# Kernel tuning notes

Hardware: AMD Instinct MI355X
Metric: run time of the kernel (lower is better)

## Reference

```python
import jax, jax.numpy as jnp
import numpy as np
from jax import lax

B, S, I = 256, 16, 64
D = 128
N_ITEMS = 100000
K = 3
PAD_ID = 0
BOS_ID = N_ITEMS
DILATIONS = (1, 2, 4)


def setup_inputs() -> dict:
    key = jax.random.key(0)
    ks = jax.random.split(key, 16)
    item_id = jax.random.randint(ks[0], (B, S, I), 0, N_ITEMS, dtype=jnp.int32)
    eval_from = jax.random.randint(ks[1], (B,), 0, S, dtype=jnp.int32)
    u_type = jax.random.randint(ks[2], (B,), 0, 4, dtype=jnp.int32)
    emb = jax.random.normal(ks[3], (N_ITEMS + 1, D), jnp.float32) * 0.05
    emb = emb.at[PAD_ID].set(0.0)  # padding_idx=0
    kaiming = (2.0 / (D * K)) ** 0.5
    conv_w0 = jax.random.normal(ks[4], (D, D, K), jnp.float32) * kaiming
    conv_w1 = jax.random.normal(ks[5], (D, D, K), jnp.float32) * kaiming
    conv_w2 = jax.random.normal(ks[6], (D, D, K), jnp.float32) * kaiming
    conv_b0 = jnp.zeros((D,), jnp.float32)
    conv_b1 = jnp.zeros((D,), jnp.float32)
    conv_b2 = jnp.zeros((D,), jnp.float32)
    gru_wih = jax.random.normal(ks[7], (3 * D, D), jnp.float32) * 0.05
    gru_whh = jax.random.normal(ks[8], (3 * D, D), jnp.float32) * 0.05
    gru_bih = jax.random.normal(ks[9], (3 * D,), jnp.float32) * 0.05
    gru_bhh = jax.random.normal(ks[10], (3 * D,), jnp.float32) * 0.05
    fus_w = jax.random.normal(ks[11], (D, 2 * D), jnp.float32) * 0.05
    fus_b = jnp.zeros((D,), jnp.float32)
    return {"item_id": item_id, "eval_from": eval_from, "u_type": u_type,
            "emb": emb,
            "conv_w0": conv_w0, "conv_b0": conv_b0,
            "conv_w1": conv_w1, "conv_b1": conv_b1,
            "conv_w2": conv_w2, "conv_b2": conv_b2,
            "gru_wih": gru_wih, "gru_whh": gru_whh,
            "gru_bih": gru_bih, "gru_bhh": gru_bhh,
            "fus_w": fus_w, "fus_b": fus_b}


def reference(item_id, eval_from, u_type, emb,
              conv_w0, conv_b0, conv_w1, conv_b1, conv_w2, conv_b2,
              gru_wih, gru_whh, gru_bih, gru_bhh, fus_w, fus_b):
    item_id = jnp.maximum(item_id, 0)  # clamp_min(0)
    Bc, Sc, Ic = item_id.shape
    convs = ((conv_w0, conv_b0, DILATIONS[0]),
             (conv_w1, conv_b1, DILATIONS[1]),
             (conv_w2, conv_b2, DILATIONS[2]))

    def tcn(x):  # x: [B, T, D] -> [B, T, D]
        h = jnp.transpose(x, (0, 2, 1))  # NCH
        for w, b, dil in convs:
            pad = (K - 1) * dil
            out = lax.conv_general_dilated(
                h, w, window_strides=(1,), padding=[(pad, 0)],
                rhs_dilation=(dil,),
                dimension_numbers=('NCH', 'OIH', 'NCH')) + b[None, :, None]
            h = jax.nn.relu(out + h)
        return jnp.transpose(h, (0, 2, 1))

    def gru_step(h, x):  # h,x: [B, D]
        gi = x @ gru_wih.T + gru_bih
        gh = h @ gru_whh.T + gru_bhh
        ir, iz, inn = jnp.split(gi, 3, axis=-1)
        hr, hz, hn = jnp.split(gh, 3, axis=-1)
        r = jax.nn.sigmoid(ir + hr)
        z = jax.nn.sigmoid(iz + hz)
        n = jnp.tanh(inn + r * hn)
        return (1.0 - z) * n + z * h

    pos = jnp.arange(Ic + 1)
    bos = jnp.full((Bc, 1), BOS_ID, dtype=item_id.dtype)

    def step(h, seq_s):  # seq_s: [B, I]
        lengths = (seq_s != PAD_ID).sum(-1)          # [B]
        max_len = lengths.max()                       # batch-level session max
        seq = jnp.concatenate([bos, seq_s], axis=1)   # [B, I+1], BOS prepended
        valid = pos[None, :] <= max_len               # positions torch keeps
        seq = jnp.where(valid, seq, PAD_ID)
        mask = seq != PAD_ID
        e = emb[seq]                                  # [B, I+1, D] (PAD row is 0)
        tc = tcn(e)
        fin = jnp.concatenate([tc, jnp.broadcast_to(h[:, None, :], tc.shape)], -1)
        reps = fin @ fus_w.T + fus_b                  # [B, I+1, D]
        reps = reps * valid[..., None]                # torch zero-pads beyond max_len
        # drop mask at last valid token (per-sample python loop in torch)
        mask = mask & ~((pos[None, :] == lengths[:, None]) & (lengths > 0)[:, None])
        mf = mask.astype(e.dtype)
        mean_emb = (e * mf[..., None]).sum(1) / jnp.maximum(mf.sum(1), 1.0)[:, None]
        h2 = gru_step(h, mean_emb)
        return h2, (reps, mask)

    h0 = jnp.zeros((Bc, D), jnp.float32)
    _, (reps, masks) = lax.scan(step, h0, jnp.transpose(item_id, (1, 0, 2)))
    reps = jnp.transpose(reps, (1, 0, 2, 3))          # [B, S, I+1, D]
    masks = jnp.transpose(masks, (1, 0, 2))           # [B, S, I+1]
    allow = jnp.arange(Sc)[None, :] >= eval_from[:, None]
    loss_masks = masks & allow[:, :, None]
    return reps, loss_masks, u_type
```

## Files before the change

### kernel.cpp

```cpp
#include <hip/hip_runtime.h>

#define BB 256
#define SS 16
#define II 64
#define DD 128
#define TT 65
#define BOS_ID 100000
#define XROW 304
#define XROWS 73
#define XT (XROWS*XROW)

#define OFF_LEN  0
#define OFF_ML   16384
#define OFF_ME   32768
#define OFF_HB   (32768 + 2097152)
#define OFF_WB2  (OFF_HB + 2097152)
#define OFF_WIHP (OFF_WB2 + 327680)
#define OFF_WGRU (OFF_WIHP + 98304)
#define OFF_GI   (OFF_WGRU + 131072)

#define OUT_MASK  (BB*SS*TT*DD)
#define OUT_UTYPE (OUT_MASK + BB*SS*TT)

typedef __attribute__((ext_vector_type(8))) short short8;
typedef __attribute__((ext_vector_type(4))) float f32x4;

__device__ __forceinline__ unsigned short f2bf(float f) {
    unsigned int u = __builtin_bit_cast(unsigned int, f);
    return (unsigned short)((u + 0x7fffu + ((u >> 16) & 1u)) >> 16);
}
__device__ __forceinline__ float bf2f(unsigned short h) {
    unsigned int u = ((unsigned int)h) << 16;
    return __builtin_bit_cast(float, u);
}
__device__ __forceinline__ void gld16(const void* g, void* l) {
    __builtin_amdgcn_global_load_lds(
        (const __attribute__((address_space(1))) void*)g,
        (__attribute__((address_space(3))) void*)l, 16, 0, 0);
}

__global__ __launch_bounds__(256) void prep_kernel(
    const float* __restrict__ w0, const float* __restrict__ w1,
    const float* __restrict__ w2, const float* __restrict__ fus_w,
    const float* __restrict__ wih, const float* __restrict__ whh,
    unsigned short* __restrict__ wB2,
    unsigned int* __restrict__ wihP, unsigned int* __restrict__ wgruP)
{
    int idx = blockIdx.x * 256 + threadIdx.x;
    if (idx < 163840) {
        int cid2  = idx >> 11;
        int inner = idx & 2047;
        int g = inner >> 9;
        int c = (inner >> 3) & 63;
        int e = inner & 7;
        int nh   = cid2 & 1;
        int rest = cid2 >> 1;
        int cq   = rest & 3;
        int m    = rest >> 2;
        int ci = cq * 32 + g * 8 + e;
        float v;
        if (m < 9) {
            int L = m / 3, k = m % 3;
            int co = nh * 64 + c;
            const float* w = (L == 0) ? w0 : ((L == 1) ? w1 : w2);
            v = w[(co * 128 + ci) * 3 + k];
        } else {
            int j = nh * 64 + c;
            v = fus_w[j * 256 + ci];
        }
        wB2[idx] = f2bf(v);
    } else if (idx < 163840 + 24576) {
        int f  = idx - 163840;
        int dd = f / 384;
        int r  = f % 384;
        unsigned int lo = f2bf(wih[r * 128 + 2 * dd]);
        unsigned int hi = f2bf(wih[r * 128 + 2 * dd + 1]);
        wihP[f] = (hi << 16) | lo;
    } else if (idx < 163840 + 24576 + 32768) {
        int f  = idx - 163840 - 24576;
        int dd = f >> 9;
        int r  = f & 511;
        float v0, v1;
        if (r < 384) { v0 = whh[r * 128 + 2 * dd]; v1 = whh[r * 128 + 2 * dd + 1]; }
        else { const float* fw = fus_w + (r - 384) * 256 + 128;
               v0 = fw[2 * dd]; v1 = fw[2 * dd + 1]; }
        wgruP[f] = ((unsigned int)f2bf(v1) << 16) | (unsigned int)f2bf(v0);
    }
}

__global__ __launch_bounds__(256) void len_kernel(
    const int* __restrict__ item_id, const int* __restrict__ u_type,
    int* __restrict__ lengths, int* __restrict__ maxlen,
    float* __restrict__ u_out)
{
    int s = blockIdx.x;
    int b = threadIdx.x;
    const int* row = item_id + (b * SS + s) * II;
    int cnt = 0;
    for (int i = 0; i < II; ++i) cnt += (row[i] > 0);
    lengths[b * SS + s] = cnt;
    __shared__ int red[256];
    red[b] = cnt;
    __syncthreads();
    for (int off = 128; off > 0; off >>= 1) {
        if (b < off) red[b] = max(red[b], red[b + off]);
        __syncthreads();
    }
    if (b == 0) maxlen[s] = red[0];
    if (s == 0) u_out[b] = (float)u_type[b];
}

__global__ __launch_bounds__(128) void mean_kernel(
    const int* __restrict__ item_id, const int* __restrict__ eval_from,
    const float* __restrict__ emb,
    const int* __restrict__ lengths, const int* __restrict__ maxlen,
    float* __restrict__ mean_emb, float* __restrict__ mask_out)
{
    int bid = blockIdx.x;
    int b = bid >> 4, s = bid & 15;
    int tid = threadIdx.x;
    __shared__ int seqs[TT];
    __shared__ int msk[TT];
    int ml  = maxlen[s];
    int len = lengths[bid];
    int ef  = eval_from[b];
    if (tid < TT) {
        int v;
        if (tid == 0) v = BOS_ID;
        else { int it = item_id[bid * II + tid - 1]; v = it > 0 ? it : 0; }
        if (tid > ml) v = 0;
        int m = (v != 0) && !(tid == len && len > 0);
        seqs[tid] = v;
        msk[tid]  = m;
        mask_out[bid * TT + tid] = (m && (s >= ef)) ? 1.0f : 0.0f;
    }
    __syncthreads();
    int cnt = 0;
    for (int p = 0; p < TT; ++p) cnt += msk[p];
    float acc = 0.0f;
    int d = tid;
    for (int p = 0; p < TT; ++p) {
        if (msk[p]) acc += emb[seqs[p] * DD + d];
    }
    mean_emb[bid * DD + d] = acc / (float)max(cnt, 1);
}

__global__ __launch_bounds__(384, 1) void gi_kernel(
    const float* __restrict__ me_all, const unsigned int* __restrict__ wihP,
    const float* __restrict__ bih, float* __restrict__ gi_all)
{
    __shared__ __align__(16) unsigned int wl[64 * 384];
    __shared__ __align__(16) float me[DD];
    int t   = threadIdx.x;
    int blk = blockIdx.x;
    {
        const unsigned char* g = (const unsigned char*)wihP + t * 16;
        unsigned char* l = (unsigned char*)wl + t * 16;
#pragma unroll
        for (int i = 0; i < 16; ++i) gld16(g + i * 6144, l + i * 6144);
    }
    float bi = bih[t];
    asm volatile("s_waitcnt vmcnt(0)" ::: "memory");
    __syncthreads();
    for (int q = 0; q < 16; ++q) {
        int bs = blk * 16 + q;
        if (t < DD) me[t] = me_all[bs * DD + t];
        __syncthreads();
        float acc = bi;
#pragma unroll
        for (int dd = 0; dd < 64; ++dd) {
            unsigned int u = wl[dd * 384 + t];
            float f0 = __builtin_bit_cast(float, u << 16);
            float f1 = __builtin_bit_cast(float, u & 0xffff0000u);
            acc += f0 * me[2 * dd] + f1 * me[2 * dd + 1];
        }
        gi_all[bs * 384 + t] = acc;
        __syncthreads();
    }
}

__global__ __launch_bounds__(512, 1) void gru_kernel(
    const unsigned int* __restrict__ wgruP, const float* __restrict__ bhh,
    const float* __restrict__ fus_b, const float* __restrict__ gi_all,
    float* __restrict__ hB)
{
    __shared__ __align__(16) unsigned int wl[64 * 512];
    __shared__ float h[DD];
    __shared__ float g_z[DD], g_inn[DD], g_hn[DD];
    int t = threadIdx.x;
    int b = blockIdx.x;
    int j = t & 127;
    int grp = t >> 7;
    {
        const unsigned char* g = (const unsigned char*)wgruP + t * 16;
        unsigned char* l = (unsigned char*)wl + t * 16;
#pragma unroll
        for (int i = 0; i < 16; ++i) gld16(g + i * 8192, l + i * 8192);
    }
    float bias = (t < 384) ? bhh[t] : fus_b[j];
    if (t < DD) h[t] = 0.0f;
    asm volatile("s_waitcnt vmcnt(0)" ::: "memory");
    __syncthreads();
    for (int s = 0; s < SS; ++s) {
        float gi = (grp < 3) ? gi_all[(b * SS + s) * 384 + t] : 0.0f;
        float acc = bias;
#pragma unroll
        for (int dd = 0; dd < 64; ++dd) {
            unsigned int u = wl[dd * 512 + t];
            float f0 = __builtin_bit_cast(float, u << 16);
            float f1 = __builtin_bit_cast(float, u & 0xffff0000u);
            acc += f0 * h[2 * dd] + f1 * h[2 * dd + 1];
        }
        if (grp == 3) {
            hB[(s * BB + b) * DD + j] = acc;
        } else if (grp == 1) { g_z[j] = gi + acc; }
        else if (grp == 2)   { g_inn[j] = gi; g_hn[j] = acc; }
        __syncthreads();
        if (grp == 0) {
            float r = 1.0f / (1.0f + expf(-(gi + acc)));
            float z = 1.0f / (1.0f + expf(-g_z[j]));
            float n = tanhf(g_inn[j] + r * g_hn[j]);
            h[j] = (1.0f - z) * n + z * h[j];
        }
        __syncthreads();
    }
}

__global__ __launch_bounds__(256, 2) void tcn_kernel(
    const int* __restrict__ item_id, const float* __restrict__ emb,
    const int* __restrict__ maxlen,
    const unsigned short* __restrict__ wB2,
    const float* __restrict__ cb0, const float* __restrict__ cb1,
    const float* __restrict__ cb2,
    const float* __restrict__ hB, float* __restrict__ reps)
{
    __shared__ __align__(16) unsigned char lds_x[2][XT];
    __shared__ __align__(16) unsigned char ring[4][2][4096];
    __shared__ int seqs2[2][TT];

    const int tid = threadIdx.x, bid = blockIdx.x;
    const int lane = tid & 63, wv = tid >> 6;
    const int l15 = lane & 15, q4 = lane >> 4;
    const int t = wv >> 1, nh = wv & 1;
    const int tile = bid * 2 + t;
    const int b = tile >> 4, s = tile & 15;
    const int ml = maxlen[s];

    const unsigned char* wsrc = (const unsigned char*)wB2 + nh * 4096 + lane * 16;
    unsigned char* xb = lds_x[t];

    {
#pragma unroll
        for (int i = 0; i < 4; ++i) gld16(wsrc + i * 1024, &ring[wv][0][i * 1024]);
#pragma unroll
        for (int i = 0; i < 4; ++i) gld16(wsrc + 8192 + i * 1024, &ring[wv][1][i * 1024]);
    }

    if (tid < 2 * TT) {
        int tt = tid / TT, p = tid - tt * TT;
        int tl = bid * 2 + tt;
        int v;
        if (p == 0) v = BOS_ID;
        else { int it = item_id[tl * II + p - 1]; v = it > 0 ? it : 0; }
        if (p > maxlen[tl & 15]) v = 0;
        seqs2[tt][p] = v;
    }
    for (int i = tid; i < 608; i += 256) {
        *(unsigned int*)(lds_x[0] + i * 4) = 0u;
        *(unsigned int*)(lds_x[1] + i * 4) = 0u;
    }
    __syncthreads();

    for (int p = nh; p < TT; p += 2) {
        const float* er = emb + (long)seqs2[t][p] * DD + lane * 2;
        float f0 = er[0], f1 = er[1];
        unsigned int pk = ((unsigned int)f2bf(f1) << 16) | (unsigned int)f2bf(f0);
        *(unsigned int*)(xb + (8 + p) * XROW + lane * 4) = pk;
    }

    float bias[3][4], hb[4];
#pragma unroll
    for (int nt = 0; nt < 4; ++nt) {
        int co = nh * 64 + nt * 16 + l15;
        bias[0][nt] = cb0[co]; bias[1][nt] = cb1[co]; bias[2][nt] = cb2[co];
        hb[nt] = hB[(s * BB + b) * DD + co];
    }
    __syncthreads();

    f32x4 acc[5][4];

#pragma unroll 1
    for (int cid = 0; cid < 40; ++cid) {
        int L = 0, cq, off, kq = 0;
        if (cid < 36) { L = cid / 12; kq = cid - L * 12; int k = kq >> 2; cq = kq & 3; off = (2 - k) << L; }
        else { cq = cid - 36; off = 0; }
        if (cid == 36 || (cid < 36 && kq == 0)) {
#pragma unroll
            for (int mt = 0; mt < 5; ++mt)
#pragma unroll
                for (int nt = 0; nt < 4; ++nt)
#pragma unroll
                    for (int r = 0; r < 4; ++r) acc[mt][nt][r] = 0.0f;
        }
        if (cid < 39) asm volatile("s_waitcnt vmcnt(4)" ::: "memory");
        else          asm volatile("s_waitcnt vmcnt(0)" ::: "memory");

        const unsigned char* sb = &ring[wv][cid & 1][0];
        short8 bfr[4], af[5];
#pragma unroll
        for (int nt = 0; nt < 4; ++nt)
            bfr[nt] = *(const short8*)(sb + q4 * 1024 + (nt * 16 + l15) * 16);
#pragma unroll
        for (int mt = 0; mt < 5; ++mt) {
            int rowA = 8 + mt * 16 + l15 - off;
            af[mt] = *(const short8*)(xb + rowA * XROW + cq * 64 + q4 * 16);
        }
        asm volatile("s_waitcnt lgkmcnt(0)" ::: "memory");
        __builtin_amdgcn_sched_barrier(0);
        if (cid <= 37) {
            const unsigned char* src = wsrc + (size_t)(cid + 2) * 8192;
#pragma unroll
            for (int i = 0; i < 4; ++i) gld16(src + i * 1024, &ring[wv][cid & 1][i * 1024]);
        }
#pragma unroll
        for (int mt = 0; mt < 5; ++mt)
#pragma unroll
            for (int nt = 0; nt < 4; ++nt)
                acc[mt][nt] = __builtin_amdgcn_mfma_f32_16x16x32_bf16(
                    af[mt], bfr[nt], acc[mt][nt], 0, 0, 0);

        if (cid < 36 && kq == 11) {
            __syncthreads();
#pragma unroll
            for (int mt = 0; mt < 5; ++mt)
#pragma unroll
                for (int nt = 0; nt < 4; ++nt) {
#pragma unroll
                    for (int r = 0; r < 4; ++r) {
                        int p = mt * 16 + q4 * 4 + r;
                        if (p < TT) {
                            int addr = (8 + p) * XROW + nh * 128 + (nt * 16 + l15) * 2;
                            float v = acc[mt][nt][r] + bias[L][nt] +
                                      bf2f(*(const unsigned short*)(xb + addr));
                            *(unsigned short*)(xb + addr) = f2bf(v > 0.f ? v : 0.f);
                        }
                    }
                }
            __syncthreads();
        }
    }

    long ob = (long)tile * (TT * DD);
#pragma unroll
    for (int mt = 0; mt < 5; ++mt)
#pragma unroll
        for (int nt = 0; nt < 4; ++nt) {
            int co = nh * 64 + nt * 16 + l15;
#pragma unroll
            for (int r = 0; r < 4; ++r) {
                int p = mt * 16 + q4 * 4 + r;
                if (p < TT) {
                    float v = (p <= ml) ? (acc[mt][nt][r] + hb[nt]) : 0.0f;
                    reps[ob + p * DD + co] = v;
                }
            }
        }
}

extern "C" void kernel_launch(void* const* d_in, const int* in_sizes, int n_in,
                              void* d_out, int out_size, void* d_ws, size_t ws_size,
                              hipStream_t stream) {
    const int*   item_id   = (const int*)  d_in[0];
    const int*   eval_from = (const int*)  d_in[1];
    const int*   u_type    = (const int*)  d_in[2];
    const float* emb       = (const float*)d_in[3];
    const float* conv_w0   = (const float*)d_in[4];
    const float* conv_b0   = (const float*)d_in[5];
    const float* conv_w1   = (const float*)d_in[6];
    const float* conv_b1   = (const float*)d_in[7];
    const float* conv_w2   = (const float*)d_in[8];
    const float* conv_b2   = (const float*)d_in[9];
    const float* gru_wih   = (const float*)d_in[10];
    const float* gru_whh   = (const float*)d_in[11];
    const float* gru_bih   = (const float*)d_in[12];
    const float* gru_bhh   = (const float*)d_in[13];
    const float* fus_w     = (const float*)d_in[14];
    const float* fus_b     = (const float*)d_in[15];

    char* ws = (char*)d_ws;
    int*            lengths  = (int*)           (ws + OFF_LEN);
    int*            maxlen   = (int*)           (ws + OFF_ML);
    float*          mean_emb = (float*)         (ws + OFF_ME);
    float*          hB       = (float*)         (ws + OFF_HB);
    unsigned short* wB2      = (unsigned short*)(ws + OFF_WB2);
    unsigned int*   wihP     = (unsigned int*)  (ws + OFF_WIHP);
    unsigned int*   wgruP    = (unsigned int*)  (ws + OFF_WGRU);
    float*          gi_all   = (float*)         (ws + OFF_GI);

    float* out  = (float*)d_out;
    float* reps = out;
    float* mout = out + OUT_MASK;
    float* uout = out + OUT_UTYPE;

    prep_kernel<<<864, 256, 0, stream>>>(conv_w0, conv_w1, conv_w2, fus_w,
                                         gru_wih, gru_whh, wB2, wihP, wgruP);
    len_kernel<<<SS, 256, 0, stream>>>(item_id, u_type, lengths, maxlen, uout);
    mean_kernel<<<BB * SS, 128, 0, stream>>>(item_id, eval_from, emb, lengths, maxlen,
                                             mean_emb, mout);
    gi_kernel<<<BB, 384, 0, stream>>>(mean_emb, wihP, gru_bih, gi_all);
    gru_kernel<<<BB, 512, 0, stream>>>(wgruP, gru_bhh, fus_b, gi_all, hB);
    tcn_kernel<<<BB * SS / 2, 256, 0, stream>>>(item_id, emb, maxlen, wB2,
                                                conv_b0, conv_b1, conv_b2, hB, reps);
}
```

Before: 269.4 us.

## Use one wave per tile with shared weight ring and folded residual

The TCN kernel now has each wave own a whole 65x128 tile instead of splitting output channels across two waves. Weight chunks are staged once per block into a 4-slot shared ring used by both waves, rather than in per-wave copies. The residual add is folded into the weights by adding identity to the k=2 tap, which removes the LDS read of the old activation during the ReLU update. The cost is twice as many accumulator registers per wave (160 floats), fewer waves per block, and a block barrier on every chunk iteration.

```diff
diff --git a/kernel.cpp b/kernel.cpp
--- a/kernel.cpp
+++ b/kernel.cpp
@@ -58,15 +58,15 @@
         int cq   = rest & 3;
         int m    = rest >> 2;
         int ci = cq * 32 + g * 8 + e;
+        int co = nh * 64 + c;
         float v;
         if (m < 9) {
             int L = m / 3, k = m % 3;
-            int co = nh * 64 + c;
             const float* w = (L == 0) ? w0 : ((L == 1) ? w1 : w2);
             v = w[(co * 128 + ci) * 3 + k];
+            if (k == 2 && ci == co) v += 1.0f;
         } else {
-            int j = nh * 64 + c;
-            v = fus_w[j * 256 + ci];
+            v = fus_w[co * 256 + ci];
         }
         wB2[idx] = f2bf(v);
     } else if (idx < 163840 + 24576) {
@@ -226,7 +226,7 @@
     }
 }
 
-__global__ __launch_bounds__(256, 2) void tcn_kernel(
+__global__ __launch_bounds__(128, 2) void tcn_kernel(
     const int* __restrict__ item_id, const float* __restrict__ emb,
     const int* __restrict__ maxlen,
     const unsigned short* __restrict__ wB2,
@@ -235,29 +235,26 @@
     const float* __restrict__ hB, float* __restrict__ reps)
 {
     __shared__ __align__(16) unsigned char lds_x[2][XT];
-    __shared__ __align__(16) unsigned char ring[4][2][4096];
+    __shared__ __align__(16) unsigned char ring[4][8192];
     __shared__ int seqs2[2][TT];
 
     const int tid = threadIdx.x, bid = blockIdx.x;
     const int lane = tid & 63, wv = tid >> 6;
     const int l15 = lane & 15, q4 = lane >> 4;
-    const int t = wv >> 1, nh = wv & 1;
-    const int tile = bid * 2 + t;
+    const int tile = bid * 2 + wv;
     const int b = tile >> 4, s = tile & 15;
-    const int ml = maxlen[s];
-
-    const unsigned char* wsrc = (const unsigned char*)wB2 + nh * 4096 + lane * 16;
-    unsigned char* xb = lds_x[t];
-
-    {
-#pragma unroll
-        for (int i = 0; i < 4; ++i) gld16(wsrc + i * 1024, &ring[wv][0][i * 1024]);
-#pragma unroll
-        for (int i = 0; i < 4; ++i) gld16(wsrc + 8192 + i * 1024, &ring[wv][1][i * 1024]);
-    }
-
-    if (tid < 2 * TT) {
-        int tt = tid / TT, p = tid - tt * TT;
+
+    const unsigned char* wbase = (const unsigned char*)wB2 + wv * 4096 + lane * 16;
+    unsigned char* xb = lds_x[wv];
+
+#pragma unroll
+    for (int slot = 0; slot < 2; ++slot)
+#pragma unroll
+        for (int i = 0; i < 4; ++i)
+            gld16(wbase + slot * 8192 + i * 1024, &ring[slot][wv * 4096 + i * 1024]);
+
+    for (int idx = tid; idx < 2 * TT; idx += 128) {
+        int tt = idx / TT, p = idx - tt * TT;
         int tl = bid * 2 + tt;
         int v;
         if (p == 0) v = BOS_ID;
@@ -265,106 +262,102 @@
         if (p > maxlen[tl & 15]) v = 0;
         seqs2[tt][p] = v;
     }
-    for (int i = tid; i < 608; i += 256) {
+    for (int i = tid; i < 608; i += 128) {
         *(unsigned int*)(lds_x[0] + i * 4) = 0u;
         *(unsigned int*)(lds_x[1] + i * 4) = 0u;
     }
     __syncthreads();
 
-    for (int p = nh; p < TT; p += 2) {
-        const float* er = emb + (long)seqs2[t][p] * DD + lane * 2;
-        float f0 = er[0], f1 = er[1];
-        unsigned int pk = ((unsigned int)f2bf(f1) << 16) | (unsigned int)f2bf(f0);
+#pragma unroll 4
+    for (int p = 0; p < TT; ++p) {
+        const float2 e = *((const float2*)(emb + (long)seqs2[wv][p] * DD) + lane);
+        unsigned int pk = ((unsigned int)f2bf(e.y) << 16) | (unsigned int)f2bf(e.x);
         *(unsigned int*)(xb + (8 + p) * XROW + lane * 4) = pk;
     }
 
-    float bias[3][4], hb[4];
-#pragma unroll
-    for (int nt = 0; nt < 4; ++nt) {
-        int co = nh * 64 + nt * 16 + l15;
-        bias[0][nt] = cb0[co]; bias[1][nt] = cb1[co]; bias[2][nt] = cb2[co];
-        hb[nt] = hB[(s * BB + b) * DD + co];
-    }
-    __syncthreads();
-
-    f32x4 acc[5][4];
+    f32x4 acc[5][8];
 
 #pragma unroll 1
     for (int cid = 0; cid < 40; ++cid) {
-        int L = 0, cq, off, kq = 0;
+        int L = 0, kq = 0, cq, off;
         if (cid < 36) { L = cid / 12; kq = cid - L * 12; int k = kq >> 2; cq = kq & 3; off = (2 - k) << L; }
         else { cq = cid - 36; off = 0; }
         if (cid == 36 || (cid < 36 && kq == 0)) {
 #pragma unroll
             for (int mt = 0; mt < 5; ++mt)
 #pragma unroll
-                for (int nt = 0; nt < 4; ++nt)
+                for (int nt = 0; nt < 8; ++nt)
 #pragma unroll
                     for (int r = 0; r < 4; ++r) acc[mt][nt][r] = 0.0f;
         }
         if (cid < 39) asm volatile("s_waitcnt vmcnt(4)" ::: "memory");
         else          asm volatile("s_waitcnt vmcnt(0)" ::: "memory");
-
-        const unsigned char* sb = &ring[wv][cid & 1][0];
-        short8 bfr[4], af[5];
-#pragma unroll
-        for (int nt = 0; nt < 4; ++nt)
-            bfr[nt] = *(const short8*)(sb + q4 * 1024 + (nt * 16 + l15) * 16);
-#pragma unroll
-        for (int mt = 0; mt < 5; ++mt) {
-            int rowA = 8 + mt * 16 + l15 - off;
-            af[mt] = *(const short8*)(xb + rowA * XROW + cq * 64 + q4 * 16);
-        }
-        asm volatile("s_waitcnt lgkmcnt(0)" ::: "memory");
-        __builtin_amdgcn_sched_barrier(0);
+        __syncthreads();
+
         if (cid <= 37) {
-            const unsigned char* src = wsrc + (size_t)(cid + 2) * 8192;
-#pragma unroll
-            for (int i = 0; i < 4; ++i) gld16(src + i * 1024, &ring[wv][cid & 1][i * 1024]);
-        }
+            const unsigned char* src = wbase + (size_t)(cid + 2) * 8192;
+            unsigned char* dst = &ring[(cid + 2) & 3][wv * 4096];
+#pragma unroll
+            for (int i = 0; i < 4; ++i) gld16(src + i * 1024, dst + i * 1024);
+        }
+
+        const unsigned char* sb = &ring[cid & 3][0];
+        short8 af[5];
 #pragma unroll
         for (int mt = 0; mt < 5; ++mt)
-#pragma unroll
-            for (int nt = 0; nt < 4; ++nt)
+            af[mt] = *(const short8*)(xb + (8 + mt * 16 + l15 - off) * XROW +
+                                      cq * 64 + q4 * 16);
+#pragma unroll
+        for (int nt = 0; nt < 8; ++nt) {
+            short8 bf = *(const short8*)(sb + (nt >> 2) * 4096 + q4 * 1024 +
+                                         ((nt & 3) * 16 + l15) * 16);
+#pragma unroll
+            for (int mt = 0; mt < 5; ++mt)
                 acc[mt][nt] = __builtin_amdgcn_mfma_f32_16x16x32_bf16(
-                    af[mt], bfr[nt], acc[mt][nt], 0, 0, 0);
+                    af[mt], bf, acc[mt][nt], 0, 0, 0);
+        }
 
         if (cid < 36 && kq == 11) {
-            __syncthreads();
-#pragma unroll
-            for (int mt = 0; mt < 5; ++mt)
-#pragma unroll
-                for (int nt = 0; nt < 4; ++nt) {
+            const float* cb = (L == 0) ? cb0 : ((L == 1) ? cb1 : cb2);
+#pragma unroll
+            for (int nt = 0; nt < 8; ++nt) {
+                float bia = cb[nt * 16 + l15];
+#pragma unroll
+                for (int mt = 0; mt < 5; ++mt)
 #pragma unroll
                     for (int r = 0; r < 4; ++r) {
                         int p = mt * 16 + q4 * 4 + r;
                         if (p < TT) {
-                            int addr = (8 + p) * XROW + nh * 128 + (nt * 16 + l15) * 2;
-                            float v = acc[mt][nt][r] + bias[L][nt] +
-                                      bf2f(*(const unsigned short*)(xb + addr));
-                            *(unsigned short*)(xb + addr) = f2bf(v > 0.f ? v : 0.f);
+                            float v = acc[mt][nt][r] + bia;
+                            *(unsigned short*)(xb + (8 + p) * XROW +
+                                               (nt * 16 + l15) * 2) =
+                                f2bf(v > 0.f ? v : 0.f);
                         }
                     }
-                }
-            __syncthreads();
-        }
-    }
-
+            }
+            asm volatile("s_waitcnt lgkmcnt(0)" ::: "memory");
+            __builtin_amdgcn_sched_barrier(0);
+        }
+    }
+
+    const int ml = maxlen[s];
+    const float* hbp = hB + (s * BB + b) * DD;
+    float hb[8];
+#pragma unroll
+    for (int nt = 0; nt < 8; ++nt) hb[nt] = hbp[nt * 16 + l15];
     long ob = (long)tile * (TT * DD);
 #pragma unroll
     for (int mt = 0; mt < 5; ++mt)
 #pragma unroll
-        for (int nt = 0; nt < 4; ++nt) {
-            int co = nh * 64 + nt * 16 + l15;
+        for (int nt = 0; nt < 8; ++nt)
 #pragma unroll
             for (int r = 0; r < 4; ++r) {
                 int p = mt * 16 + q4 * 4 + r;
                 if (p < TT) {
                     float v = (p <= ml) ? (acc[mt][nt][r] + hb[nt]) : 0.0f;
-                    reps[ob + p * DD + co] = v;
+                    reps[ob + p * DD + nt * 16 + l15] = v;
                 }
             }
-        }
 }
 
 extern "C" void kernel_launch(void* const* d_in, const int* in_sizes, int n_in,
@@ -409,6 +402,6 @@
                                              mean_emb, mout);
     gi_kernel<<<BB, 384, 0, stream>>>(mean_emb, wihP, gru_bih, gi_all);
     gru_kernel<<<BB, 512, 0, stream>>>(wgruP, gru_bhh, fus_b, gi_all, hB);
-    tcn_kernel<<<BB * SS / 2, 256, 0, stream>>>(item_id, emb, maxlen, wB2,
+    tcn_kernel<<<BB * SS / 2, 128, 0, stream>>>(item_id, emb, maxlen, wB2,
                                                 conv_b0, conv_b1, conv_b2, hB, reps);
 }
```

After: 451.6 us. +67.6%, slower.

## Fold residual into conv weights, XOR-swizzle LDS, shrink ring to raise occupancy

Applied to the files above, without the earlier changes.

The residual add is folded into the last conv tap's weights (identity added in prep), so the epilogue no longer reads the old activation from LDS. The activation tile drops its row padding and uses an XOR swizzle to avoid bank conflicts. The per-wave weight ring is replaced by a block-shared double buffer that now also holds the sequence ids, and bias and hidden values are loaded late to save registers. Together these cut LDS use so launch bounds can rise to 3 blocks per CU. The cost is a full vmcnt(0) wait plus a block barrier on every chunk, and the residual now passes through bf16 weights, which can change rounding.

```diff
diff --git a/kernel.cpp b/kernel.cpp
--- a/kernel.cpp
+++ b/kernel.cpp
@@ -6,7 +6,7 @@
 #define DD 128
 #define TT 65
 #define BOS_ID 100000
-#define XROW 304
+#define XROW 256
 #define XROWS 73
 #define XT (XROWS*XROW)
 
@@ -28,10 +28,6 @@
 __device__ __forceinline__ unsigned short f2bf(float f) {
     unsigned int u = __builtin_bit_cast(unsigned int, f);
     return (unsigned short)((u + 0x7fffu + ((u >> 16) & 1u)) >> 16);
-}
-__device__ __forceinline__ float bf2f(unsigned short h) {
-    unsigned int u = ((unsigned int)h) << 16;
-    return __builtin_bit_cast(float, u);
 }
 __device__ __forceinline__ void gld16(const void* g, void* l) {
     __builtin_amdgcn_global_load_lds(
@@ -58,15 +54,15 @@
         int cq   = rest & 3;
         int m    = rest >> 2;
         int ci = cq * 32 + g * 8 + e;
+        int co = nh * 64 + c;
         float v;
         if (m < 9) {
             int L = m / 3, k = m % 3;
-            int co = nh * 64 + c;
             const float* w = (L == 0) ? w0 : ((L == 1) ? w1 : w2);
             v = w[(co * 128 + ci) * 3 + k];
+            if (k == 2 && ci == co) v += 1.0f;
         } else {
-            int j = nh * 64 + c;
-            v = fus_w[j * 256 + ci];
+            v = fus_w[co * 256 + ci];
         }
         wB2[idx] = f2bf(v);
     } else if (idx < 163840 + 24576) {
@@ -226,7 +222,7 @@
     }
 }
 
-__global__ __launch_bounds__(256, 2) void tcn_kernel(
+__global__ __launch_bounds__(256, 3) void tcn_kernel(
     const int* __restrict__ item_id, const float* __restrict__ emb,
     const int* __restrict__ maxlen,
     const unsigned short* __restrict__ wB2,
@@ -235,8 +231,7 @@
     const float* __restrict__ hB, float* __restrict__ reps)
 {
     __shared__ __align__(16) unsigned char lds_x[2][XT];
-    __shared__ __align__(16) unsigned char ring[4][2][4096];
-    __shared__ int seqs2[2][TT];
+    __shared__ __align__(16) unsigned char ring[2][8192];
 
     const int tid = threadIdx.x, bid = blockIdx.x;
     const int lane = tid & 63, wv = tid >> 6;
@@ -246,16 +241,15 @@
     const int b = tile >> 4, s = tile & 15;
     const int ml = maxlen[s];
 
-    const unsigned char* wsrc = (const unsigned char*)wB2 + nh * 4096 + lane * 16;
+    const unsigned char* wgbase = (const unsigned char*)wB2;
     unsigned char* xb = lds_x[t];
 
     {
-#pragma unroll
-        for (int i = 0; i < 4; ++i) gld16(wsrc + i * 1024, &ring[wv][0][i * 1024]);
-#pragma unroll
-        for (int i = 0; i < 4; ++i) gld16(wsrc + 8192 + i * 1024, &ring[wv][1][i * 1024]);
-    }
-
+        const unsigned char* src = wgbase + wv * 1024 + lane * 16;
+        gld16(src,        &ring[0][wv * 1024]);
+        gld16(src + 4096, &ring[0][4096 + wv * 1024]);
+    }
+    int* seqs2 = (int*)&ring[1][0];
     if (tid < 2 * TT) {
         int tt = tid / TT, p = tid - tt * TT;
         int tl = bid * 2 + tt;
@@ -263,29 +257,21 @@
         if (p == 0) v = BOS_ID;
         else { int it = item_id[tl * II + p - 1]; v = it > 0 ? it : 0; }
         if (p > maxlen[tl & 15]) v = 0;
-        seqs2[tt][p] = v;
-    }
-    for (int i = tid; i < 608; i += 256) {
-        *(unsigned int*)(lds_x[0] + i * 4) = 0u;
-        *(unsigned int*)(lds_x[1] + i * 4) = 0u;
+        seqs2[tt * TT + p] = v;
+    }
+    {
+        float4 z = {0.f, 0.f, 0.f, 0.f};
+        if (tid < 128) *(float4*)(lds_x[0] + tid * 16) = z;
+        else           *(float4*)(lds_x[1] + (tid - 128) * 16) = z;
     }
     __syncthreads();
 
     for (int p = nh; p < TT; p += 2) {
-        const float* er = emb + (long)seqs2[t][p] * DD + lane * 2;
+        const float* er = emb + (long)seqs2[t * TT + p] * DD + lane * 2;
         float f0 = er[0], f1 = er[1];
         unsigned int pk = ((unsigned int)f2bf(f1) << 16) | (unsigned int)f2bf(f0);
-        *(unsigned int*)(xb + (8 + p) * XROW + lane * 4) = pk;
-    }
-
-    float bias[3][4], hb[4];
-#pragma unroll
-    for (int nt = 0; nt < 4; ++nt) {
-        int co = nh * 64 + nt * 16 + l15;
-        bias[0][nt] = cb0[co]; bias[1][nt] = cb1[co]; bias[2][nt] = cb2[co];
-        hb[nt] = hB[(s * BB + b) * DD + co];
-    }
-    __syncthreads();
+        *(unsigned int*)(xb + (8 + p) * XROW + ((lane * 4) ^ ((p & 7) << 4))) = pk;
+    }
 
     f32x4 acc[5][4];
 
@@ -302,10 +288,19 @@
 #pragma unroll
                     for (int r = 0; r < 4; ++r) acc[mt][nt][r] = 0.0f;
         }
-        if (cid < 39) asm volatile("s_waitcnt vmcnt(4)" ::: "memory");
-        else          asm volatile("s_waitcnt vmcnt(0)" ::: "memory");
-
-        const unsigned char* sb = &ring[wv][cid & 1][0];
+        asm volatile("s_waitcnt vmcnt(0)" ::: "memory");
+        __syncthreads();
+
+        if (cid <= 38) {
+            const unsigned char* src =
+                wgbase + (size_t)(cid + 1) * 8192 + wv * 1024 + lane * 16;
+            gld16(src,        &ring[(cid + 1) & 1][wv * 1024]);
+            gld16(src + 4096, &ring[(cid + 1) & 1][4096 + wv * 1024]);
+        }
+
+        const unsigned char* sb = &ring[cid & 1][nh * 4096];
+        const int xmask = ((l15 - off) & 7) << 4;
+        const int colx  = (cq * 64 + q4 * 16) ^ xmask;
         short8 bfr[4], af[5];
 #pragma unroll
         for (int nt = 0; nt < 4; ++nt)
@@ -313,58 +308,57 @@
 #pragma unroll
         for (int mt = 0; mt < 5; ++mt) {
             int rowA = 8 + mt * 16 + l15 - off;
-            af[mt] = *(const short8*)(xb + rowA * XROW + cq * 64 + q4 * 16);
-        }
-        asm volatile("s_waitcnt lgkmcnt(0)" ::: "memory");
-        __builtin_amdgcn_sched_barrier(0);
-        if (cid <= 37) {
-            const unsigned char* src = wsrc + (size_t)(cid + 2) * 8192;
-#pragma unroll
-            for (int i = 0; i < 4; ++i) gld16(src + i * 1024, &ring[wv][cid & 1][i * 1024]);
-        }
-#pragma unroll
-        for (int mt = 0; mt < 5; ++mt)
-#pragma unroll
-            for (int nt = 0; nt < 4; ++nt)
+            af[mt] = *(const short8*)(xb + rowA * XROW + colx);
+        }
+#pragma unroll
+        for (int nt = 0; nt < 4; ++nt)
+#pragma unroll
+            for (int mt = 0; mt < 5; ++mt)
                 acc[mt][nt] = __builtin_amdgcn_mfma_f32_16x16x32_bf16(
                     af[mt], bfr[nt], acc[mt][nt], 0, 0, 0);
 
         if (cid < 36 && kq == 11) {
+            const float* cb = (L == 0) ? cb0 : ((L == 1) ? cb1 : cb2);
             __syncthreads();
 #pragma unroll
-            for (int mt = 0; mt < 5; ++mt)
-#pragma unroll
-                for (int nt = 0; nt < 4; ++nt) {
+            for (int nt = 0; nt < 4; ++nt) {
+                float bia = cb[nh * 64 + nt * 16 + l15];
+                int cbyte = nh * 128 + nt * 32 + l15 * 2;
+#pragma unroll
+                for (int mt = 0; mt < 5; ++mt)
 #pragma unroll
                     for (int r = 0; r < 4; ++r) {
                         int p = mt * 16 + q4 * 4 + r;
                         if (p < TT) {
-                            int addr = (8 + p) * XROW + nh * 128 + (nt * 16 + l15) * 2;
-                            float v = acc[mt][nt][r] + bias[L][nt] +
-                                      bf2f(*(const unsigned short*)(xb + addr));
-                            *(unsigned short*)(xb + addr) = f2bf(v > 0.f ? v : 0.f);
+                            int row = 8 + p;
+                            float v = acc[mt][nt][r] + bia;
+                            *(unsigned short*)(xb + row * XROW +
+                                               (cbyte ^ ((row & 7) << 4))) =
+                                f2bf(v > 0.f ? v : 0.f);
                         }
                     }
-                }
+            }
             __syncthreads();
         }
     }
 
+    float hb[4];
+#pragma unroll
+    for (int nt = 0; nt < 4; ++nt)
+        hb[nt] = hB[(s * BB + b) * DD + nh * 64 + nt * 16 + l15];
     long ob = (long)tile * (TT * DD);
 #pragma unroll
     for (int mt = 0; mt < 5; ++mt)
 #pragma unroll
-        for (int nt = 0; nt < 4; ++nt) {
-            int co = nh * 64 + nt * 16 + l15;
+        for (int nt = 0; nt < 4; ++nt)
 #pragma unroll
             for (int r = 0; r < 4; ++r) {
                 int p = mt * 16 + q4 * 4 + r;
                 if (p < TT) {
                     float v = (p <= ml) ? (acc[mt][nt][r] + hb[nt]) : 0.0f;
-                    reps[ob + p * DD + co] = v;
+                    reps[ob + p * DD + nh * 64 + nt * 16 + l15] = v;
                 }
             }
-        }
 }
 
 extern "C" void kernel_launch(void* const* d_in, const int* in_sizes, int n_in,
```

After: 267.5 us. No clear change (-0.7%).
